# Kernel tuning notes

Measured on AMD Instinct MI355X. Metric: run time of the kernel, lower is better.

The kernel has to match this reference:

```python
import jax, jax.numpy as jnp
import numpy as np


def setup_inputs() -> dict:
    key = jax.random.key(0)
    k0, k1, k2, k3 = jax.random.split(key, 4)
    T, H, I, E = 2048, 2048, 5632, 8
    return {
        "hidden_states": jax.random.normal(k0, (T, H), dtype=jnp.float32),
        "gate_w": jax.random.normal(k1, (E, H), dtype=jnp.float32) * 0.02,
        "w1": jax.random.normal(k2, (E, 2 * I, H), dtype=jnp.float32) * 0.02,
        "w2": jax.random.normal(k3, (E, H, I), dtype=jnp.float32) * 0.02,
        "top_k": 2,
    }


def reference(hidden_states, gate_w, w1, w2, top_k):
    # hidden_states: [T, H]; gate_w: [E, H]; w1: [E, 2I, H]; w2: [E, H, I]
    T = hidden_states.shape[0]
    E = w1.shape[0]
    router_logits = hidden_states @ gate_w.T                    # [T, E]
    probs = jax.nn.softmax(router_logits, axis=-1)
    topk_w, topk_idx = jax.lax.top_k(probs, top_k)              # [T, k]
    # renormalize=False in fused_moe: use raw softmax top-k weights.
    # Dense combine matrix C[t, e] = weight of expert e for token t (0 if unrouted).
    combine = jnp.zeros((T, E), dtype=probs.dtype)
    combine = combine.at[jnp.arange(T)[:, None], topk_idx].add(topk_w)
    out = jnp.zeros_like(hidden_states)
    for e in range(E):  # small fixed expert loop
        gate_up = hidden_states @ w1[e].T                       # [T, 2I]
        g, u = jnp.split(gate_up, 2, axis=-1)
        h = jax.nn.silu(g) * u                                  # SiluAndMul
        out = out + combine[:, e:e + 1] * (h @ w2[e].T)         # [T, H]
    return out
```

## Files before the change

### kernel.cpp

```cpp
#include <hip/hip_runtime.h>
#include <hip/hip_bf16.h>

typedef __bf16 bf16_t;
typedef __bf16 bf16x4 __attribute__((ext_vector_type(4)));
typedef __bf16 bf16x8 __attribute__((ext_vector_type(8)));
typedef float  f32x4  __attribute__((ext_vector_type(4)));

constexpr int T_ = 2048, H_ = 2048, I_ = 5632, E_ = 8, S_ = T_ * 2;

constexpr size_t OFF_HB    = 0;
constexpr size_t OFF_HOUT  = OFF_HB    + (size_t)T_ * H_ * 2;
constexpr size_t OFF_DPART = OFF_HOUT  + (size_t)S_ * I_ * 2;
constexpr size_t OFF_TOS   = OFF_DPART + (size_t)S_ * H_ * 4;
constexpr size_t OFF_SOT   = OFF_TOS   + (size_t)S_ * 4;
constexpr size_t OFF_TKI   = OFF_SOT   + (size_t)S_ * 4;
constexpr size_t OFF_TKW   = OFF_TKI   + (size_t)S_ * 4;
constexpr size_t OFF_CNT   = OFF_TKW   + (size_t)S_ * 4;
constexpr size_t OFF_OFFS  = OFF_CNT   + 64;
constexpr size_t OFF_CUR   = OFF_OFFS  + 64;
constexpr size_t OFF_HG    = OFF_CUR   + 64;

__device__ __forceinline__ void gload16(const void* g, void* l) {
  __builtin_amdgcn_global_load_lds(
      (const __attribute__((address_space(1))) void*)g,
      (__attribute__((address_space(3))) void*)l, 16, 0, 0);
}

__device__ __forceinline__ void gld4(f32x4& d, const float* p) {
  asm volatile("global_load_dwordx4 %0, %1, off" : "=&v"(d) : "v"(p) : "memory");
}

__device__ __forceinline__ bf16x4 cvt4v(f32x4 a) {
  bf16x4 r; r[0]=(bf16_t)a[0]; r[1]=(bf16_t)a[1]; r[2]=(bf16_t)a[2]; r[3]=(bf16_t)a[3];
  return r;
}

#define SBAR() do { __builtin_amdgcn_s_barrier(); __builtin_amdgcn_sched_barrier(0); } while (0)
#define WAITV(N) do { asm volatile("s_waitcnt vmcnt(" #N ")" ::: "memory"); \
                      __builtin_amdgcn_sched_barrier(0); } while (0)
#define WAITL0() do { asm volatile("s_waitcnt lgkmcnt(0)" ::: "memory"); \
                      __builtin_amdgcn_sched_barrier(0); } while (0)

__global__ __launch_bounds__(256)
void router_kernel(const float* __restrict__ hs, const float* __restrict__ gw,
                   int* __restrict__ tki, float* __restrict__ tkw,
                   int* __restrict__ counts, bf16_t* __restrict__ hb)
{
  const int t = blockIdx.x;
  const int tid = threadIdx.x;
  const int lane = tid & 63, wid = tid >> 6;
  const float* hrow = hs + (size_t)t * H_;
  const int c0 = tid * 8;
  float4 h0 = *(const float4*)(hrow + c0);
  float4 h1 = *(const float4*)(hrow + c0 + 4);
  bf16x8 hv;
  hv[0]=(bf16_t)h0.x; hv[1]=(bf16_t)h0.y; hv[2]=(bf16_t)h0.z; hv[3]=(bf16_t)h0.w;
  hv[4]=(bf16_t)h1.x; hv[5]=(bf16_t)h1.y; hv[6]=(bf16_t)h1.z; hv[7]=(bf16_t)h1.w;
  *(bf16x8*)(hb + (size_t)t * H_ + c0) = hv;

  float acc[E_];
  #pragma unroll
  for (int e = 0; e < E_; ++e) {
    const float* g = gw + (size_t)e * H_ + c0;
    float4 g0 = *(const float4*)(g);
    float4 g1 = *(const float4*)(g + 4);
    acc[e] = h0.x*g0.x + h0.y*g0.y + h0.z*g0.z + h0.w*g0.w
           + h1.x*g1.x + h1.y*g1.y + h1.z*g1.z + h1.w*g1.w;
  }
  #pragma unroll
  for (int e = 0; e < E_; ++e)
    #pragma unroll
    for (int o = 32; o > 0; o >>= 1)
      acc[e] += __shfl_down(acc[e], o);
  __shared__ float red[4][E_];
  if (lane == 0)
    #pragma unroll
    for (int e = 0; e < E_; ++e) red[wid][e] = acc[e];
  __syncthreads();
  if (tid == 0) {
    float l[E_];
    #pragma unroll
    for (int e = 0; e < E_; ++e) l[e] = red[0][e] + red[1][e] + red[2][e] + red[3][e];
    float m = l[0];
    #pragma unroll
    for (int e = 1; e < E_; ++e) m = fmaxf(m, l[e]);
    float p[E_]; float s = 0.f;
    #pragma unroll
    for (int e = 0; e < E_; ++e) { p[e] = __expf(l[e] - m); s += p[e]; }
    int i1 = 0;
    #pragma unroll
    for (int e = 1; e < E_; ++e) if (l[e] > l[i1]) i1 = e;
    int i2 = (i1 == 0) ? 1 : 0;
    #pragma unroll
    for (int e = 0; e < E_; ++e) if (e != i1 && l[e] > l[i2]) i2 = e;
    tki[2*t] = i1; tki[2*t+1] = i2;
    tkw[2*t] = p[i1] / s; tkw[2*t+1] = p[i2] / s;
    atomicAdd(&counts[i1], 1);
    atomicAdd(&counts[i2], 1);
  }
}

__global__ void scan_kernel(const int* __restrict__ counts, const int* __restrict__ tki,
                            int* __restrict__ offs, int* __restrict__ cursor,
                            int* __restrict__ tos, int* __restrict__ sot)
{
  if (threadIdx.x == 0) {
    int run = 0;
    for (int e = 0; e < E_; ++e) { offs[e] = run; cursor[e] = run; run += counts[e]; }
  }
  __syncthreads();
  for (int t = threadIdx.x; t < T_; t += blockDim.x) {
    #pragma unroll
    for (int k = 0; k < 2; ++k) {
      int e = tki[2*t + k];
      int s = atomicAdd(&cursor[e], 1);
      tos[s] = t;
      sot[2*t + k] = s;
    }
  }
}

__global__ __launch_bounds__(256)
void gather_kernel(const bf16_t* __restrict__ hb, const int* __restrict__ tos,
                   bf16_t* __restrict__ hg)
{
  const int slot = blockIdx.x;
  const int tok  = tos[slot];
  const int c = threadIdx.x * 8;
  *(bf16x8*)(hg + (size_t)slot * H_ + c) = *(const bf16x8*)(hb + (size_t)tok * H_ + c);
}

constexpr int G1_ABUF = 16384, G1_BBUF = 8192;
constexpr int G1_BBASE = 3 * G1_ABUF;

__global__ __launch_bounds__(512, 4)
void gemm1_kernel(const bf16_t* __restrict__ hg, const float* __restrict__ w1,
                  const int* __restrict__ offs, const int* __restrict__ counts,
                  bf16_t* __restrict__ hout)
{
  const int bid = blockIdx.x;
  const int e   = bid & 7;
  const int idx = bid >> 3;
  const int mt  = idx & 3;
  const int nt  = idx >> 2;

  const int cnt = counts[e];
  const int m0 = mt * 256;
  if (m0 >= cnt) return;
  const int off = offs[e];
  const int n0 = nt * 64;

  const float* Wg = w1 + (size_t)e * (2 * (size_t)I_ * H_) + (size_t)n0 * H_;

  __shared__ char smem[3 * G1_ABUF + 2 * G1_BBUF];

  const int tid = threadIdx.x;
  const int lane = tid & 63, wid = tid >> 6;
  const int wm = wid >> 1, wn = wid & 1;
  const int l15 = lane & 15, l4 = lane >> 4;

  const bf16_t* agp[2]; int aoff[2];
  #pragma unroll
  for (int i = 0; i < 2; ++i) {
    int q = wid * 2 + i;
    int w = (lane & 7) ^ ((lane >> 3) & 7);
    int row = 2 * (q * 8 + (lane >> 3)) + (w >> 2);
    int slot = off + m0 + row, mx = off + cnt - 1;
    if (slot > mx) slot = mx;
    agp[i]  = hg + (size_t)slot * H_ + (w & 3) * 8;
    aoff[i] = q * 1024;
  }
  auto stageA = [&](int ab, int t) {
    char* p = smem + ab * G1_ABUF;
    #pragma unroll
    for (int i = 0; i < 2; ++i) gload16(agp[i] + t * 32, p + aoff[i]);
  };

  const int brow = tid >> 3, bseg = tid & 7;
  const float* bgsrc = Wg + (size_t)brow * H_ + bseg * 4;
  const float* busrc = Wg + (size_t)(I_ + brow) * H_ + bseg * 4;
  int gOff, uOff;
  {
    int ng = brow, nu = 64 + brow;
    int wg_ = (ng & 1) * 4 + (bseg >> 1), wu_ = (nu & 1) * 4 + (bseg >> 1);
    gOff = (ng >> 1) * 128 + (wg_ ^ ((ng >> 1) & 7)) * 16 + (bseg & 1) * 8;
    uOff = (nu >> 1) * 128 + (wu_ ^ ((nu >> 1) & 7)) * 16 + (bseg & 1) * 8;
  }
  f32x4 b0g, b0u, b1g, b1u;

  f32x4 accg[4][2], accu[4][2];
  #pragma unroll
  for (int mi = 0; mi < 4; ++mi)
    #pragma unroll
    for (int ni = 0; ni < 2; ++ni) {
      accg[mi][ni] = f32x4{0.f,0.f,0.f,0.f};
      accu[mi][ni] = f32x4{0.f,0.f,0.f,0.f};
    }

  const int phys = ((((l15 & 1) << 2) | l4) ^ ((l15 >> 1) & 7)) * 16;

  auto compute = [&](int ab, int blds) {
    const char* ap = smem + ab * G1_ABUF;
    const char* bp2 = smem + G1_BBASE + blds * G1_BBUF;
    bf16x8 bgf[2], buf2[2];
    #pragma unroll
    for (int ni = 0; ni < 2; ++ni) {
      int pb = wn * 16 + ni * 8 + (l15 >> 1);
      bgf[ni]  = *(const bf16x8*)(bp2 + pb * 128 + phys);
      buf2[ni] = *(const bf16x8*)(bp2 + (pb + 32) * 128 + phys);
    }
    #pragma unroll
    for (int mi = 0; mi < 4; ++mi) {
      int pr = wm * 32 + mi * 8 + (l15 >> 1);
      bf16x8 af = *(const bf16x8*)(ap + pr * 128 + phys);
      accg[mi][0] = __builtin_amdgcn_mfma_f32_16x16x32_bf16(af, bgf[0],  accg[mi][0], 0, 0, 0);
      accg[mi][1] = __builtin_amdgcn_mfma_f32_16x16x32_bf16(af, bgf[1],  accg[mi][1], 0, 0, 0);
      accu[mi][0] = __builtin_amdgcn_mfma_f32_16x16x32_bf16(af, buf2[0], accu[mi][0], 0, 0, 0);
      accu[mi][1] = __builtin_amdgcn_mfma_f32_16x16x32_bf16(af, buf2[1], accu[mi][1], 0, 0, 0);
    }
  };
  auto writeB = [&](int blds, f32x4& g, f32x4& u) {
    char* bp2 = smem + G1_BBASE + blds * G1_BBUF;
    *(bf16x4*)(bp2 + gOff) = cvt4v(g);
    *(bf16x4*)(bp2 + uOff) = cvt4v(u);
  };

  constexpr int NK = H_ / 32;
  stageA(0, 0);
  gld4(b0g, bgsrc); gld4(b0u, busrc);
  stageA(1, 1);
  gld4(b1g, bgsrc + 32); gld4(b1u, busrc + 32);
  WAITV(4);
  writeB(0, b0g, b0u);
  WAITL0();
  SBAR();

  int aR = 0, aN = 1, aW = 2;
  for (int t = 0; t < NK - 2; t += 2) {
    stageA(aW, t + 2);
    gld4(b0g, bgsrc + (t + 2) * 32); gld4(b0u, busrc + (t + 2) * 32);
    compute(aR, 0);
    WAITV(4);
    writeB(1, b1g, b1u);
    WAITL0();
    SBAR();
    { int tmp = aR; aR = aN; aN = aW; aW = tmp; }
    stageA(aW, t + 3);
    gld4(b1g, bgsrc + (t + 3) * 32); gld4(b1u, busrc + (t + 3) * 32);
    compute(aR, 1);
    WAITV(4);
    writeB(0, b0g, b0u);
    WAITL0();
    SBAR();
    { int tmp = aR; aR = aN; aN = aW; aW = tmp; }
  }
  compute(aR, 0);
  WAITV(0);
  writeB(1, b1g, b1u);
  WAITL0();
  SBAR();
  compute(aN, 1);

  #pragma unroll
  for (int mi = 0; mi < 4; ++mi)
    #pragma unroll
    for (int ni = 0; ni < 2; ++ni)
      #pragma unroll
      for (int j = 0; j < 4; ++j) {
        int rel = wm*64 + mi*16 + l4*4 + j;
        if (m0 + rel < cnt) {
          int col = n0 + wn*32 + ni*16 + l15;
          float g = accg[mi][ni][j];
          float u = accu[mi][ni][j];
          float hvv = (g / (1.0f + __expf(-g))) * u;
          hout[(size_t)(off + m0 + rel) * I_ + col] = (bf16_t)hvv;
        }
      }
}

constexpr int G2_ABUF = 16384, G2_BBUF = 4096;
constexpr int G2_BBASE = 3 * G2_ABUF;

__global__ __launch_bounds__(512, 4)
void gemm2_kernel(const bf16_t* __restrict__ hbuf, const float* __restrict__ w2,
                  const int* __restrict__ offs, const int* __restrict__ counts,
                  float* __restrict__ dpart)
{
  const int bid = blockIdx.x;
  const int e   = bid & 7;
  const int idx = bid >> 3;
  const int mt  = idx & 3;
  const int nt  = idx >> 2;

  const int cnt = counts[e];
  const int m0 = mt * 256;
  if (m0 >= cnt) return;
  const int off = offs[e];
  const int n0 = nt * 64;
  const float* W = w2 + (size_t)e * ((size_t)H_ * I_) + (size_t)n0 * I_;

  __shared__ char smem[3 * G2_ABUF + 2 * G2_BBUF];

  const int tid = threadIdx.x;
  const int lane = tid & 63, wid = tid >> 6;
  const int wm = wid >> 1, wn = wid & 1;
  const int l15 = lane & 15, l4 = lane >> 4;

  const bf16_t* agp[2]; int aoff[2];
  #pragma unroll
  for (int i = 0; i < 2; ++i) {
    int q = wid * 2 + i;
    int w = (lane & 7) ^ ((lane >> 3) & 7);
    int row = 2 * (q * 8 + (lane >> 3)) + (w >> 2);
    int slot = off + m0 + row, mx = off + cnt - 1;
    if (slot > mx) slot = mx;
    agp[i]  = hbuf + (size_t)slot * I_ + (w & 3) * 8;
    aoff[i] = q * 1024;
  }
  auto stageA = [&](int ab, int t) {
    char* p = smem + ab * G2_ABUF;
    #pragma unroll
    for (int i = 0; i < 2; ++i) gload16(agp[i] + t * 32, p + aoff[i]);
  };

  const int brow = tid >> 3, bseg = tid & 7;
  const float* bsrc = W + (size_t)brow * I_ + bseg * 4;
  int bOff;
  {
    int w_ = (brow & 1) * 4 + (bseg >> 1);
    bOff = (brow >> 1) * 128 + (w_ ^ ((brow >> 1) & 7)) * 16 + (bseg & 1) * 8;
  }
  f32x4 b0, b1;

  f32x4 acc[4][2];
  #pragma unroll
  for (int mi = 0; mi < 4; ++mi)
    #pragma unroll
    for (int ni = 0; ni < 2; ++ni) acc[mi][ni] = f32x4{0.f,0.f,0.f,0.f};

  const int phys = ((((l15 & 1) << 2) | l4) ^ ((l15 >> 1) & 7)) * 16;

  auto compute = [&](int ab, int blds) {
    const char* ap = smem + ab * G2_ABUF;
    const char* bp2 = smem + G2_BBASE + blds * G2_BBUF;
    bf16x8 bf[2];
    #pragma unroll
    for (int ni = 0; ni < 2; ++ni) {
      int pb = wn * 16 + ni * 8 + (l15 >> 1);
      bf[ni] = *(const bf16x8*)(bp2 + pb * 128 + phys);
    }
    #pragma unroll
    for (int mi = 0; mi < 4; ++mi) {
      int pr = wm * 32 + mi * 8 + (l15 >> 1);
      bf16x8 af = *(const bf16x8*)(ap + pr * 128 + phys);
      acc[mi][0] = __builtin_amdgcn_mfma_f32_16x16x32_bf16(af, bf[0], acc[mi][0], 0, 0, 0);
      acc[mi][1] = __builtin_amdgcn_mfma_f32_16x16x32_bf16(af, bf[1], acc[mi][1], 0, 0, 0);
    }
  };
  auto writeB = [&](int blds, f32x4& v) {
    *(bf16x4*)(smem + G2_BBASE + blds * G2_BBUF + bOff) = cvt4v(v);
  };

  constexpr int NK = I_ / 32;
  stageA(0, 0);
  gld4(b0, bsrc);
  stageA(1, 1);
  gld4(b1, bsrc + 32);
  WAITV(3);
  writeB(0, b0);
  WAITL0();
  SBAR();

  int aR = 0, aN = 1, aW = 2;
  for (int t = 0; t < NK - 2; t += 2) {
    stageA(aW, t + 2);
    gld4(b0, bsrc + (t + 2) * 32);
    compute(aR, 0);
    WAITV(3);
    writeB(1, b1);
    WAITL0();
    SBAR();
    { int tmp = aR; aR = aN; aN = aW; aW = tmp; }
    stageA(aW, t + 3);
    gld4(b1, bsrc + (t + 3) * 32);
    compute(aR, 1);
    WAITV(3);
    writeB(0, b0);
    WAITL0();
    SBAR();
    { int tmp = aR; aR = aN; aN = aW; aW = tmp; }
  }
  compute(aR, 0);
  WAITV(0);
  writeB(1, b1);
  WAITL0();
  SBAR();
  compute(aN, 1);

  #pragma unroll
  for (int mi = 0; mi < 4; ++mi)
    #pragma unroll
    for (int ni = 0; ni < 2; ++ni)
      #pragma unroll
      for (int j = 0; j < 4; ++j) {
        int rel = wm*64 + mi*16 + l4*4 + j;
        if (m0 + rel < cnt) {
          int col = n0 + wn*32 + ni*16 + l15;
          dpart[(size_t)(off + m0 + rel) * H_ + col] = acc[mi][ni][j];
        }
      }
}

__global__ __launch_bounds__(256)
void combine_kernel(const float* __restrict__ dpart, const int* __restrict__ sot,
                    const float* __restrict__ tkw, float* __restrict__ out)
{
  int idx = blockIdx.x * 256 + threadIdx.x;
  int t = idx >> 9;
  int c = (idx & 511) * 4;
  float wA = tkw[2*t], wB = tkw[2*t+1];
  int sA = sot[2*t], sB = sot[2*t+1];
  float4 a = *(const float4*)(dpart + (size_t)sA * H_ + c);
  float4 b = *(const float4*)(dpart + (size_t)sB * H_ + c);
  float4 o;
  o.x = wA*a.x + wB*b.x; o.y = wA*a.y + wB*b.y;
  o.z = wA*a.z + wB*b.z; o.w = wA*a.w + wB*b.w;
  *(float4*)(out + (size_t)t * H_ + c) = o;
}

extern "C" void kernel_launch(void* const* d_in, const int* in_sizes, int n_in,
                              void* d_out, int out_size, void* d_ws, size_t ws_size,
                              hipStream_t stream) {
  const float* hs = (const float*)d_in[0];
  const float* gw = (const float*)d_in[1];
  const float* w1 = (const float*)d_in[2];
  const float* w2 = (const float*)d_in[3];
  float* out = (float*)d_out;
  char* ws = (char*)d_ws;

  bf16_t* hb    = (bf16_t*)(ws + OFF_HB);
  bf16_t* hout  = (bf16_t*)(ws + OFF_HOUT);
  float*  dpart = (float*) (ws + OFF_DPART);
  int*    tos   = (int*)   (ws + OFF_TOS);
  int*    sot   = (int*)   (ws + OFF_SOT);
  int*    tki   = (int*)   (ws + OFF_TKI);
  float*  tkw   = (float*) (ws + OFF_TKW);
  int*    cnt   = (int*)   (ws + OFF_CNT);
  int*    offp  = (int*)   (ws + OFF_OFFS);
  int*    curp  = (int*)   (ws + OFF_CUR);
  bf16_t* hg    = (bf16_t*)(ws + OFF_HG);

  hipMemsetAsync(ws + OFF_CNT, 0, 64, stream);

  router_kernel<<<T_, 256, 0, stream>>>(hs, gw, tki, tkw, cnt, hb);
  scan_kernel<<<1, 256, 0, stream>>>(cnt, tki, offp, curp, tos, sot);
  gather_kernel<<<S_, 256, 0, stream>>>(hb, tos, hg);
  gemm1_kernel<<<4 * (2 * I_ / 128) * E_, 512, 0, stream>>>(hg, w1, offp, cnt, hout);
  gemm2_kernel<<<4 * (H_ / 64) * E_, 512, 0, stream>>>(hout, w2, offp, cnt, dpart);
  combine_kernel<<<(T_ * H_ / 4) / 256, 256, 0, stream>>>(dpart, sot, tkw, out);
}
```

Baseline: 971.7 us.

## Double the N tile of both expert GEMMs to 128 columns

Both grouped GEMM kernels now compute 128-column output tiles instead of 64. gemm1 gives each warp 8×2 gate and up accumulators, and gemm2 gives each warp 4×4. The B-loading path is reorganised so each thread converts wider fp32 weight chunks to bf16 and writes them to LDS with 8-wide stores. The aim is to halve how often the activation tiles are re-streamed and to raise MFMA work per LDS read. In exchange, register use roughly doubles, occupancy drops to 2 blocks per CU, and the grid gets fewer blocks.

```diff
diff --git a/kernel.cpp b/kernel.cpp
--- a/kernel.cpp
+++ b/kernel.cpp
@@ -30,8 +30,10 @@
   asm volatile("global_load_dwordx4 %0, %1, off" : "=&v"(d) : "v"(p) : "memory");
 }
 
-__device__ __forceinline__ bf16x4 cvt4v(f32x4 a) {
-  bf16x4 r; r[0]=(bf16_t)a[0]; r[1]=(bf16_t)a[1]; r[2]=(bf16_t)a[2]; r[3]=(bf16_t)a[3];
+__device__ __forceinline__ bf16x8 cvt8(f32x4 a, f32x4 b) {
+  bf16x8 r;
+  r[0]=(bf16_t)a[0]; r[1]=(bf16_t)a[1]; r[2]=(bf16_t)a[2]; r[3]=(bf16_t)a[3];
+  r[4]=(bf16_t)b[0]; r[5]=(bf16_t)b[1]; r[6]=(bf16_t)b[2]; r[7]=(bf16_t)b[3];
   return r;
 }
 
@@ -130,10 +132,10 @@
   *(bf16x8*)(hg + (size_t)slot * H_ + c) = *(const bf16x8*)(hb + (size_t)tok * H_ + c);
 }
 
-constexpr int G1_ABUF = 16384, G1_BBUF = 8192;
+constexpr int G1_ABUF = 16384, G1_BBUF = 16384;
 constexpr int G1_BBASE = 3 * G1_ABUF;
 
-__global__ __launch_bounds__(512, 4)
+__global__ __launch_bounds__(512, 2)
 void gemm1_kernel(const bf16_t* __restrict__ hg, const float* __restrict__ w1,
                   const int* __restrict__ offs, const int* __restrict__ counts,
                   bf16_t* __restrict__ hout)
@@ -148,7 +150,7 @@
   const int m0 = mt * 256;
   if (m0 >= cnt) return;
   const int off = offs[e];
-  const int n0 = nt * 64;
+  const int n0 = nt * 128;
 
   const float* Wg = w1 + (size_t)e * (2 * (size_t)I_ * H_) + (size_t)n0 * H_;
 
@@ -156,7 +158,7 @@
 
   const int tid = threadIdx.x;
   const int lane = tid & 63, wid = tid >> 6;
-  const int wm = wid >> 1, wn = wid & 1;
+  const int wm = wid >> 2, wn = wid & 3;
   const int l15 = lane & 15, l4 = lane >> 4;
 
   const bf16_t* agp[2]; int aoff[2];
@@ -176,21 +178,21 @@
     for (int i = 0; i < 2; ++i) gload16(agp[i] + t * 32, p + aoff[i]);
   };
 
-  const int brow = tid >> 3, bseg = tid & 7;
-  const float* bgsrc = Wg + (size_t)brow * H_ + bseg * 4;
-  const float* busrc = Wg + (size_t)(I_ + brow) * H_ + bseg * 4;
-  int gOff, uOff;
+  const int brow = tid >> 1, bh = tid & 1;
+  const size_t bwrow = (brow < 128) ? (size_t)brow : (size_t)(I_ + brow - 128);
+  const float* bsrc = Wg + bwrow * H_ + bh * 16;
+  int bOff0, bOff1;
   {
-    int ng = brow, nu = 64 + brow;
-    int wg_ = (ng & 1) * 4 + (bseg >> 1), wu_ = (nu & 1) * 4 + (bseg >> 1);
-    gOff = (ng >> 1) * 128 + (wg_ ^ ((ng >> 1) & 7)) * 16 + (bseg & 1) * 8;
-    uOff = (nu >> 1) * 128 + (wu_ ^ ((nu >> 1) & 7)) * 16 + (bseg & 1) * 8;
-  }
-  f32x4 b0g, b0u, b1g, b1u;
-
-  f32x4 accg[4][2], accu[4][2];
-  #pragma unroll
-  for (int mi = 0; mi < 4; ++mi)
+    int p = brow >> 1, sub = brow & 1;
+    int w0 = sub * 4 + bh * 2, w1_ = w0 + 1;
+    bOff0 = p * 128 + ((w0  ^ (p & 7)) * 16);
+    bOff1 = p * 128 + ((w1_ ^ (p & 7)) * 16);
+  }
+  f32x4 b0a, b0b, b0c, b0d, b1a, b1b, b1c, b1d;
+
+  f32x4 accg[8][2], accu[8][2];
+  #pragma unroll
+  for (int mi = 0; mi < 8; ++mi)
     #pragma unroll
     for (int ni = 0; ni < 2; ++ni) {
       accg[mi][ni] = f32x4{0.f,0.f,0.f,0.f};
@@ -201,17 +203,17 @@
 
   auto compute = [&](int ab, int blds) {
     const char* ap = smem + ab * G1_ABUF;
-    const char* bp2 = smem + G1_BBASE + blds * G1_BBUF;
+    const char* bp = smem + G1_BBASE + blds * G1_BBUF;
     bf16x8 bgf[2], buf2[2];
     #pragma unroll
     for (int ni = 0; ni < 2; ++ni) {
-      int pb = wn * 16 + ni * 8 + (l15 >> 1);
-      bgf[ni]  = *(const bf16x8*)(bp2 + pb * 128 + phys);
-      buf2[ni] = *(const bf16x8*)(bp2 + (pb + 32) * 128 + phys);
-    }
-    #pragma unroll
-    for (int mi = 0; mi < 4; ++mi) {
-      int pr = wm * 32 + mi * 8 + (l15 >> 1);
+      int rg = wn * 32 + ni * 16 + l15;
+      bgf[ni]  = *(const bf16x8*)(bp + (rg >> 1) * 128 + phys);
+      buf2[ni] = *(const bf16x8*)(bp + ((rg + 128) >> 1) * 128 + phys);
+    }
+    #pragma unroll
+    for (int mi = 0; mi < 8; ++mi) {
+      int pr = wm * 64 + mi * 8 + (l15 >> 1);
       bf16x8 af = *(const bf16x8*)(ap + pr * 128 + phys);
       accg[mi][0] = __builtin_amdgcn_mfma_f32_16x16x32_bf16(af, bgf[0],  accg[mi][0], 0, 0, 0);
       accg[mi][1] = __builtin_amdgcn_mfma_f32_16x16x32_bf16(af, bgf[1],  accg[mi][1], 0, 0, 0);
@@ -219,55 +221,57 @@
       accu[mi][1] = __builtin_amdgcn_mfma_f32_16x16x32_bf16(af, buf2[1], accu[mi][1], 0, 0, 0);
     }
   };
-  auto writeB = [&](int blds, f32x4& g, f32x4& u) {
-    char* bp2 = smem + G1_BBASE + blds * G1_BBUF;
-    *(bf16x4*)(bp2 + gOff) = cvt4v(g);
-    *(bf16x4*)(bp2 + uOff) = cvt4v(u);
+  auto writeB = [&](int blds, f32x4& a, f32x4& b, f32x4& c, f32x4& d) {
+    char* bp = smem + G1_BBASE + blds * G1_BBUF;
+    *(bf16x8*)(bp + bOff0) = cvt8(a, b);
+    *(bf16x8*)(bp + bOff1) = cvt8(c, d);
   };
 
   constexpr int NK = H_ / 32;
   stageA(0, 0);
-  gld4(b0g, bgsrc); gld4(b0u, busrc);
+  gld4(b0a, bsrc); gld4(b0b, bsrc + 4); gld4(b0c, bsrc + 8); gld4(b0d, bsrc + 12);
   stageA(1, 1);
-  gld4(b1g, bgsrc + 32); gld4(b1u, busrc + 32);
-  WAITV(4);
-  writeB(0, b0g, b0u);
+  gld4(b1a, bsrc + 32); gld4(b1b, bsrc + 36); gld4(b1c, bsrc + 40); gld4(b1d, bsrc + 44);
+  WAITV(6);
+  writeB(0, b0a, b0b, b0c, b0d);
   WAITL0();
   SBAR();
 
   int aR = 0, aN = 1, aW = 2;
   for (int t = 0; t < NK - 2; t += 2) {
     stageA(aW, t + 2);
-    gld4(b0g, bgsrc + (t + 2) * 32); gld4(b0u, busrc + (t + 2) * 32);
+    { const float* s = bsrc + (t + 2) * 32;
+      gld4(b0a, s); gld4(b0b, s + 4); gld4(b0c, s + 8); gld4(b0d, s + 12); }
     compute(aR, 0);
-    WAITV(4);
-    writeB(1, b1g, b1u);
+    WAITV(6);
+    writeB(1, b1a, b1b, b1c, b1d);
     WAITL0();
     SBAR();
     { int tmp = aR; aR = aN; aN = aW; aW = tmp; }
     stageA(aW, t + 3);
-    gld4(b1g, bgsrc + (t + 3) * 32); gld4(b1u, busrc + (t + 3) * 32);
+    { const float* s = bsrc + (t + 3) * 32;
+      gld4(b1a, s); gld4(b1b, s + 4); gld4(b1c, s + 8); gld4(b1d, s + 12); }
     compute(aR, 1);
-    WAITV(4);
-    writeB(0, b0g, b0u);
+    WAITV(6);
+    writeB(0, b0a, b0b, b0c, b0d);
     WAITL0();
     SBAR();
     { int tmp = aR; aR = aN; aN = aW; aW = tmp; }
   }
   compute(aR, 0);
   WAITV(0);
-  writeB(1, b1g, b1u);
+  writeB(1, b1a, b1b, b1c, b1d);
   WAITL0();
   SBAR();
   compute(aN, 1);
 
   #pragma unroll
-  for (int mi = 0; mi < 4; ++mi)
+  for (int mi = 0; mi < 8; ++mi)
     #pragma unroll
     for (int ni = 0; ni < 2; ++ni)
       #pragma unroll
       for (int j = 0; j < 4; ++j) {
-        int rel = wm*64 + mi*16 + l4*4 + j;
+        int rel = wm*128 + mi*16 + l4*4 + j;
         if (m0 + rel < cnt) {
           int col = n0 + wn*32 + ni*16 + l15;
           float g = accg[mi][ni][j];
@@ -278,10 +282,10 @@
       }
 }
 
-constexpr int G2_ABUF = 16384, G2_BBUF = 4096;
+constexpr int G2_ABUF = 16384, G2_BBUF = 8192;
 constexpr int G2_BBASE = 3 * G2_ABUF;
 
-__global__ __launch_bounds__(512, 4)
+__global__ __launch_bounds__(512, 2)
 void gemm2_kernel(const bf16_t* __restrict__ hbuf, const float* __restrict__ w2,
                   const int* __restrict__ offs, const int* __restrict__ counts,
                   float* __restrict__ dpart)
@@ -296,7 +300,7 @@
   const int m0 = mt * 256;
   if (m0 >= cnt) return;
   const int off = offs[e];
-  const int n0 = nt * 64;
+  const int n0 = nt * 128;
   const float* W = w2 + (size_t)e * ((size_t)H_ * I_) + (size_t)n0 * I_;
 
   __shared__ char smem[3 * G2_ABUF + 2 * G2_BBUF];
@@ -323,31 +327,32 @@
     for (int i = 0; i < 2; ++i) gload16(agp[i] + t * 32, p + aoff[i]);
   };
 
-  const int brow = tid >> 3, bseg = tid & 7;
-  const float* bsrc = W + (size_t)brow * I_ + bseg * 4;
+  const int brow = tid >> 2, bs = tid & 3;
+  const float* bsrc = W + (size_t)brow * I_ + bs * 8;
   int bOff;
   {
-    int w_ = (brow & 1) * 4 + (bseg >> 1);
-    bOff = (brow >> 1) * 128 + (w_ ^ ((brow >> 1) & 7)) * 16 + (bseg & 1) * 8;
-  }
-  f32x4 b0, b1;
-
-  f32x4 acc[4][2];
+    int p = brow >> 1, sub = brow & 1;
+    int w_ = sub * 4 + bs;
+    bOff = p * 128 + ((w_ ^ (p & 7)) * 16);
+  }
+  f32x4 b0a, b0b, b1a, b1b;
+
+  f32x4 acc[4][4];
   #pragma unroll
   for (int mi = 0; mi < 4; ++mi)
     #pragma unroll
-    for (int ni = 0; ni < 2; ++ni) acc[mi][ni] = f32x4{0.f,0.f,0.f,0.f};
+    for (int ni = 0; ni < 4; ++ni) acc[mi][ni] = f32x4{0.f,0.f,0.f,0.f};
 
   const int phys = ((((l15 & 1) << 2) | l4) ^ ((l15 >> 1) & 7)) * 16;
 
   auto compute = [&](int ab, int blds) {
     const char* ap = smem + ab * G2_ABUF;
-    const char* bp2 = smem + G2_BBASE + blds * G2_BBUF;
-    bf16x8 bf[2];
-    #pragma unroll
-    for (int ni = 0; ni < 2; ++ni) {
-      int pb = wn * 16 + ni * 8 + (l15 >> 1);
-      bf[ni] = *(const bf16x8*)(bp2 + pb * 128 + phys);
+    const char* bp = smem + G2_BBASE + blds * G2_BBUF;
+    bf16x8 bf[4];
+    #pragma unroll
+    for (int ni = 0; ni < 4; ++ni) {
+      int r = wn * 64 + ni * 16 + l15;
+      bf[ni] = *(const bf16x8*)(bp + (r >> 1) * 128 + phys);
     }
     #pragma unroll
     for (int mi = 0; mi < 4; ++mi) {
@@ -355,44 +360,46 @@
       bf16x8 af = *(const bf16x8*)(ap + pr * 128 + phys);
       acc[mi][0] = __builtin_amdgcn_mfma_f32_16x16x32_bf16(af, bf[0], acc[mi][0], 0, 0, 0);
       acc[mi][1] = __builtin_amdgcn_mfma_f32_16x16x32_bf16(af, bf[1], acc[mi][1], 0, 0, 0);
-    }
-  };
-  auto writeB = [&](int blds, f32x4& v) {
-    *(bf16x4*)(smem + G2_BBASE + blds * G2_BBUF + bOff) = cvt4v(v);
+      acc[mi][2] = __builtin_amdgcn_mfma_f32_16x16x32_bf16(af, bf[2], acc[mi][2], 0, 0, 0);
+      acc[mi][3] = __builtin_amdgcn_mfma_f32_16x16x32_bf16(af, bf[3], acc[mi][3], 0, 0, 0);
+    }
+  };
+  auto writeB = [&](int blds, f32x4& a, f32x4& b) {
+    *(bf16x8*)(smem + G2_BBASE + blds * G2_BBUF + bOff) = cvt8(a, b);
   };
 
   constexpr int NK = I_ / 32;
   stageA(0, 0);
-  gld4(b0, bsrc);
+  gld4(b0a, bsrc); gld4(b0b, bsrc + 4);
   stageA(1, 1);
-  gld4(b1, bsrc + 32);
-  WAITV(3);
-  writeB(0, b0);
+  gld4(b1a, bsrc + 32); gld4(b1b, bsrc + 36);
+  WAITV(4);
+  writeB(0, b0a, b0b);
   WAITL0();
   SBAR();
 
   int aR = 0, aN = 1, aW = 2;
   for (int t = 0; t < NK - 2; t += 2) {
     stageA(aW, t + 2);
-    gld4(b0, bsrc + (t + 2) * 32);
+    { const float* s = bsrc + (t + 2) * 32; gld4(b0a, s); gld4(b0b, s + 4); }
     compute(aR, 0);
-    WAITV(3);
-    writeB(1, b1);
+    WAITV(4);
+    writeB(1, b1a, b1b);
     WAITL0();
     SBAR();
     { int tmp = aR; aR = aN; aN = aW; aW = tmp; }
     stageA(aW, t + 3);
-    gld4(b1, bsrc + (t + 3) * 32);
+    { const float* s = bsrc + (t + 3) * 32; gld4(b1a, s); gld4(b1b, s + 4); }
     compute(aR, 1);
-    WAITV(3);
-    writeB(0, b0);
+    WAITV(4);
+    writeB(0, b0a, b0b);
     WAITL0();
     SBAR();
     { int tmp = aR; aR = aN; aN = aW; aW = tmp; }
   }
   compute(aR, 0);
   WAITV(0);
-  writeB(1, b1);
+  writeB(1, b1a, b1b);
   WAITL0();
   SBAR();
   compute(aN, 1);
@@ -400,12 +407,12 @@
   #pragma unroll
   for (int mi = 0; mi < 4; ++mi)
     #pragma unroll
-    for (int ni = 0; ni < 2; ++ni)
+    for (int ni = 0; ni < 4; ++ni)
       #pragma unroll
       for (int j = 0; j < 4; ++j) {
         int rel = wm*64 + mi*16 + l4*4 + j;
         if (m0 + rel < cnt) {
-          int col = n0 + wn*32 + ni*16 + l15;
+          int col = n0 + wn*64 + ni*16 + l15;
           dpart[(size_t)(off + m0 + rel) * H_ + col] = acc[mi][ni][j];
         }
       }
@@ -455,7 +462,7 @@
   router_kernel<<<T_, 256, 0, stream>>>(hs, gw, tki, tkw, cnt, hb);
   scan_kernel<<<1, 256, 0, stream>>>(cnt, tki, offp, curp, tos, sot);
   gather_kernel<<<S_, 256, 0, stream>>>(hb, tos, hg);
-  gemm1_kernel<<<4 * (2 * I_ / 128) * E_, 512, 0, stream>>>(hg, w1, offp, cnt, hout);
-  gemm2_kernel<<<4 * (H_ / 64) * E_, 512, 0, stream>>>(hout, w2, offp, cnt, dpart);
+  gemm1_kernel<<<4 * (I_ / 128) * E_, 512, 0, stream>>>(hg, w1, offp, cnt, hout);
+  gemm2_kernel<<<4 * (H_ / 128) * E_, 512, 0, stream>>>(hout, w2, offp, cnt, dpart);
   combine_kernel<<<(T_ * H_ / 4) / 256, 256, 0, stream>>>(dpart, sot, tkw, out);
 }
```

New measurement: 957.8 us. About the same (-1.4%).
